# Optimization experiments

Measured on AMD Instinct MI355X. Metric: run time of the kernel, lower is better.

## Reference

```python
import jax, jax.numpy as jnp
import numpy as np

B, T, I, H, O = 2048, 512, 5, 64, 1


def setup_inputs() -> dict:
    key = jax.random.key(0)
    ks = jax.random.split(key, 11)
    s_ih0 = 1.0 / np.sqrt(H)
    def u(k, shape):
        return jax.random.uniform(k, shape, jnp.float32, -s_ih0, s_ih0)
    return {
        "x": jax.random.normal(ks[0], (B, T, I), jnp.float32),
        "W_ih0": u(ks[1], (H, I)),
        "W_hh0": u(ks[2], (H, H)),
        "b_ih0": u(ks[3], (H,)),
        "b_hh0": u(ks[4], (H,)),
        "W_ih1": u(ks[5], (H, H)),
        "W_hh1": u(ks[6], (H, H)),
        "b_ih1": u(ks[7], (H,)),
        "b_hh1": u(ks[8], (H,)),
        "fc_W": u(ks[9], (O, H)),
        "fc_b": u(ks[10], (O,)),
    }


def reference(x, W_ih0, W_hh0, b_ih0, b_hh0, W_ih1, W_hh1, b_ih1, b_hh1, fc_W, fc_b):
    # PyTorch RNN (tanh): h_t = tanh(x_t @ W_ih^T + b_ih + h_{t-1} @ W_hh^T + b_hh)
    # 2 stacked layers, h0 = zeros. Only last-timestep layer-2 output feeds fc.
    xT = jnp.swapaxes(x, 0, 1)  # [T, B, I]
    h0 = jnp.zeros((x.shape[0], H), x.dtype)

    def step(carry, x_t):
        h1, h2 = carry
        h1 = jnp.tanh(x_t @ W_ih0.T + b_ih0 + h1 @ W_hh0.T + b_hh0)
        h2 = jnp.tanh(h1 @ W_ih1.T + b_ih1 + h2 @ W_hh1.T + b_hh1)
        return (h1, h2), None

    (h1, h2), _ = jax.lax.scan(step, (h0, h0), xT)
    # out[:, -1, :] == final hidden state of top layer
    return h2 @ fc_W.T + fc_b
```

## Files before the change

kernel.cpp:

```cpp
#include <hip/hip_runtime.h>


constexpr int Bn = 2048;
constexpr int Tn = 512;
constexpr int In = 5;
constexpr int Hn = 64;

typedef _Float16 half4 __attribute__((ext_vector_type(4)));
typedef float f32x4 __attribute__((ext_vector_type(4)));

#define MFMA16(A, B, C) __builtin_amdgcn_mfma_f32_16x16x16f16((A), (B), (C), 0, 0, 0)

__device__ __forceinline__ unsigned pk(float a, float b) {
    union { _Float16 h[2]; unsigned u; } z;
    z.h[0] = (_Float16)a; z.h[1] = (_Float16)b;
    return z.u;
}
__device__ __forceinline__ half4 mkh4(unsigned a, unsigned b) {
    union { unsigned u[2]; half4 h; } z; z.u[0] = a; z.u[1] = b; return z.h;
}
__device__ __forceinline__ half4 h4of(unsigned long long v) {
    union { unsigned long long q; half4 h; } z; z.q = v; return z.h;
}

__device__ __forceinline__ float fast_tanh(float v) {
    v = __builtin_amdgcn_fmed3f(v, -15.f, 15.f);
    float e = __builtin_amdgcn_exp2f(v * 2.885390082f);
    return (e - 1.f) * __builtin_amdgcn_rcpf(e + 1.f);
}

__global__ __launch_bounds__(256) void rnn2_mfma4(
    const float* __restrict__ x,
    const float* __restrict__ W_ih0, const float* __restrict__ W_hh0,
    const float* __restrict__ b_ih0, const float* __restrict__ b_hh0,
    const float* __restrict__ W_ih1, const float* __restrict__ W_hh1,
    const float* __restrict__ b_ih1, const float* __restrict__ b_hh1,
    const float* __restrict__ fc_W, const float* __restrict__ fc_b,
    float* __restrict__ out)
{
    const int tid = threadIdx.x;
    const int w = tid >> 6;
    const int l = tid & 63;
    const int q = l >> 4, c = l & 15;
    const int b0 = blockIdx.x * 16;
    const int row = w * 16 + c;

    __shared__ unsigned long long h1buf[2][4][64];
    __shared__ unsigned long long h2buf[2][4][64];
    __shared__ float fcpart[4][16];

    half4 A_ih0;
    {
        unsigned a0 = 0, a1 = 0;
        const float* p = W_ih0 + row * In;
        if (q == 0)      { a0 = pk(p[0], p[1]); a1 = pk(p[2], p[3]); }
        else if (q == 1) { a0 = pk(p[4], 0.f); }
        A_ih0 = mkh4(a0, a1);
    }
    half4 A_hh0[4], A_ih1[4], A_hh1[4];
    #pragma unroll
    for (int kt = 0; kt < 4; ++kt) {
        const int off = row * Hn + kt * 16 + q * 4;
        float4 v0 = *reinterpret_cast<const float4*>(W_hh0 + off);
        A_hh0[kt] = mkh4(pk(v0.x, v0.y), pk(v0.z, v0.w));
        float4 v1 = *reinterpret_cast<const float4*>(W_ih1 + off);
        A_ih1[kt] = mkh4(pk(v1.x, v1.y), pk(v1.z, v1.w));
        float4 v2 = *reinterpret_cast<const float4*>(W_hh1 + off);
        A_hh1[kt] = mkh4(pk(v2.x, v2.y), pk(v2.z, v2.w));
    }

    f32x4 bc1, bc2;
    #pragma unroll
    for (int r = 0; r < 4; ++r) {
        const int rr = w * 16 + q * 4 + r;
        bc1[r] = b_ih0[rr] + b_hh0[rr];
        bc2[r] = b_ih1[rr] + b_hh1[rr];
    }

    unsigned long long h1B[4] = {0, 0, 0, 0};
    unsigned long long h2B[4] = {0, 0, 0, 0};
    f32x4 h2v = {0.f, 0.f, 0.f, 0.f};

    const float* xrow = x + (size_t)(b0 + c) * Tn * In;
    float nx0 = 0.f, nx1 = 0.f, nx2 = 0.f, nx3 = 0.f, nx4 = 0.f;
    if (q == 0)      { nx0 = xrow[0]; nx1 = xrow[1]; nx2 = xrow[2]; nx3 = xrow[3]; }
    else if (q == 1) { nx4 = xrow[4]; }

    #pragma unroll 1
    for (int t = 0; t < Tn; ++t) {
        unsigned r0 = (q == 0) ? pk(nx0, nx1) : ((q == 1) ? pk(nx4, 0.f) : 0u);
        unsigned r1 = (q == 0) ? pk(nx2, nx3) : 0u;
        const half4 XF = mkh4(r0, r1);

        const int tn = (t + 1 < Tn) ? (t + 1) : (Tn - 1);
        const float* xp = xrow + tn * In;
        if (q == 0)      { nx0 = xp[0]; nx1 = xp[1]; nx2 = xp[2]; nx3 = xp[3]; }
        else if (q == 1) { nx4 = xp[4]; }

        f32x4 acc = bc1;
        acc = MFMA16(A_ih0, XF, acc);
        #pragma unroll
        for (int kt = 0; kt < 4; ++kt)
            acc = MFMA16(A_hh0[kt], h4of(h1B[kt]), acc);
        float t0 = fast_tanh(acc[0]), t1 = fast_tanh(acc[1]);
        float t2 = fast_tanh(acc[2]), t3 = fast_tanh(acc[3]);
        unsigned long long myh1 =
            (unsigned long long)pk(t0, t1) | ((unsigned long long)pk(t2, t3) << 32);

        h1buf[t & 1][w][l] = myh1;
        __syncthreads();
        #pragma unroll
        for (int kt = 0; kt < 4; ++kt) h1B[kt] = h1buf[t & 1][kt][l];

        f32x4 aA = bc2;
        f32x4 aB = {0.f, 0.f, 0.f, 0.f};
        #pragma unroll
        for (int kt = 0; kt < 4; ++kt) {
            aA = MFMA16(A_ih1[kt], h4of(h1B[kt]), aA);
            aB = MFMA16(A_hh1[kt], h4of(h2B[kt]), aB);
        }
        h2v[0] = fast_tanh(aA[0] + aB[0]); h2v[1] = fast_tanh(aA[1] + aB[1]);
        h2v[2] = fast_tanh(aA[2] + aB[2]); h2v[3] = fast_tanh(aA[3] + aB[3]);
        unsigned long long myh2 =
            (unsigned long long)pk(h2v[0], h2v[1]) | ((unsigned long long)pk(h2v[2], h2v[3]) << 32);

        h2buf[t & 1][w][l] = myh2;
        __syncthreads();
        #pragma unroll
        for (int kt = 0; kt < 4; ++kt) h2B[kt] = h2buf[t & 1][kt][l];
    }

    float s = 0.f;
    #pragma unroll
    for (int e = 0; e < 4; ++e)
        s += fc_W[w * 16 + q * 4 + e] * h2v[e];
    s += __shfl_xor(s, 16, 64);
    s += __shfl_xor(s, 32, 64);
    if (l < 16) fcpart[w][l] = s;
    __syncthreads();
    if (tid < 16)
        out[b0 + tid] = fcpart[0][tid] + fcpart[1][tid] + fcpart[2][tid]
                      + fcpart[3][tid] + fc_b[0];
}

extern "C" void kernel_launch(void* const* d_in, const int* in_sizes, int n_in,
                              void* d_out, int out_size, void* d_ws, size_t ws_size,
                              hipStream_t stream) {
    const float* x     = (const float*)d_in[0];
    const float* W_ih0 = (const float*)d_in[1];
    const float* W_hh0 = (const float*)d_in[2];
    const float* b_ih0 = (const float*)d_in[3];
    const float* b_hh0 = (const float*)d_in[4];
    const float* W_ih1 = (const float*)d_in[5];
    const float* W_hh1 = (const float*)d_in[6];
    const float* b_ih1 = (const float*)d_in[7];
    const float* b_hh1 = (const float*)d_in[8];
    const float* fc_W  = (const float*)d_in[9];
    const float* fc_b  = (const float*)d_in[10];
    float* out = (float*)d_out;

    dim3 grid(Bn / 16);
    dim3 block(256);
    hipLaunchKernelGGL(rnn2_mfma4, grid, block, 0, stream,
                       x, W_ih0, W_hh0, b_ih0, b_hh0,
                       W_ih1, W_hh1, b_ih1, b_hh1, fc_W, fc_b, out);
}
```

Before: 360.9 us.

## Pipeline the two RNN layers across separate wave groups with one barrier per step

Splits each 512-thread block into two groups of four waves. One group computes layer 1 at step t while the other computes layer 2 at step t-1, so the two layers run concurrently with one barrier per iteration instead of two. MFMA accumulation chains are also split into independent partial sums to shorten the dependency chain. The cost is double the waves per block, an extra iteration, and divergent branches. Each block now holds twice as many threads, which may reduce how many blocks fit per CU.

```diff
diff --git a/kernel.cpp b/kernel.cpp
--- a/kernel.cpp
+++ b/kernel.cpp
@@ -29,7 +29,7 @@
     return (e - 1.f) * __builtin_amdgcn_rcpf(e + 1.f);
 }
 
-__global__ __launch_bounds__(256) void rnn2_mfma4(
+__global__ __launch_bounds__(512, 1) void rnn2_pipe(
     const float* __restrict__ x,
     const float* __restrict__ W_ih0, const float* __restrict__ W_hh0,
     const float* __restrict__ b_ih0, const float* __restrict__ b_hh0,
@@ -43,38 +43,49 @@
     const int l = tid & 63;
     const int q = l >> 4, c = l & 15;
     const int b0 = blockIdx.x * 16;
-    const int row = w * 16 + c;
+    const bool isL1 = (w < 4);
+    const int m = w & 3;
+    const int row = m * 16 + c;
 
     __shared__ unsigned long long h1buf[2][4][64];
     __shared__ unsigned long long h2buf[2][4][64];
     __shared__ float fcpart[4][16];
 
-    half4 A_ih0;
-    {
+    half4 A0 = mkh4(0u, 0u);
+    half4 AH[4], AI[4];
+    f32x4 bc;
+    if (isL1) {
         unsigned a0 = 0, a1 = 0;
         const float* p = W_ih0 + row * In;
         if (q == 0)      { a0 = pk(p[0], p[1]); a1 = pk(p[2], p[3]); }
         else if (q == 1) { a0 = pk(p[4], 0.f); }
-        A_ih0 = mkh4(a0, a1);
-    }
-    half4 A_hh0[4], A_ih1[4], A_hh1[4];
-    #pragma unroll
-    for (int kt = 0; kt < 4; ++kt) {
-        const int off = row * Hn + kt * 16 + q * 4;
-        float4 v0 = *reinterpret_cast<const float4*>(W_hh0 + off);
-        A_hh0[kt] = mkh4(pk(v0.x, v0.y), pk(v0.z, v0.w));
-        float4 v1 = *reinterpret_cast<const float4*>(W_ih1 + off);
-        A_ih1[kt] = mkh4(pk(v1.x, v1.y), pk(v1.z, v1.w));
-        float4 v2 = *reinterpret_cast<const float4*>(W_hh1 + off);
-        A_hh1[kt] = mkh4(pk(v2.x, v2.y), pk(v2.z, v2.w));
-    }
-
-    f32x4 bc1, bc2;
-    #pragma unroll
-    for (int r = 0; r < 4; ++r) {
-        const int rr = w * 16 + q * 4 + r;
-        bc1[r] = b_ih0[rr] + b_hh0[rr];
-        bc2[r] = b_ih1[rr] + b_hh1[rr];
+        A0 = mkh4(a0, a1);
+        #pragma unroll
+        for (int kt = 0; kt < 4; ++kt) {
+            const int off = row * Hn + kt * 16 + q * 4;
+            float4 v0 = *reinterpret_cast<const float4*>(W_hh0 + off);
+            AH[kt] = mkh4(pk(v0.x, v0.y), pk(v0.z, v0.w));
+            AI[kt] = mkh4(0u, 0u);
+        }
+        #pragma unroll
+        for (int r = 0; r < 4; ++r) {
+            const int rr = m * 16 + q * 4 + r;
+            bc[r] = b_ih0[rr] + b_hh0[rr];
+        }
+    } else {
+        #pragma unroll
+        for (int kt = 0; kt < 4; ++kt) {
+            const int off = row * Hn + kt * 16 + q * 4;
+            float4 v1 = *reinterpret_cast<const float4*>(W_ih1 + off);
+            AI[kt] = mkh4(pk(v1.x, v1.y), pk(v1.z, v1.w));
+            float4 v2 = *reinterpret_cast<const float4*>(W_hh1 + off);
+            AH[kt] = mkh4(pk(v2.x, v2.y), pk(v2.z, v2.w));
+        }
+        #pragma unroll
+        for (int r = 0; r < 4; ++r) {
+            const int rr = m * 16 + q * 4 + r;
+            bc[r] = b_ih1[rr] + b_hh1[rr];
+        }
     }
 
     unsigned long long h1B[4] = {0, 0, 0, 0};
@@ -83,60 +94,78 @@
 
     const float* xrow = x + (size_t)(b0 + c) * Tn * In;
     float nx0 = 0.f, nx1 = 0.f, nx2 = 0.f, nx3 = 0.f, nx4 = 0.f;
-    if (q == 0)      { nx0 = xrow[0]; nx1 = xrow[1]; nx2 = xrow[2]; nx3 = xrow[3]; }
-    else if (q == 1) { nx4 = xrow[4]; }
+    if (isL1) {
+        if (q == 0)      { nx0 = xrow[0]; nx1 = xrow[1]; nx2 = xrow[2]; nx3 = xrow[3]; }
+        else if (q == 1) { nx4 = xrow[4]; }
+    }
+
+    const f32x4 zero = {0.f, 0.f, 0.f, 0.f};
 
     #pragma unroll 1
-    for (int t = 0; t < Tn; ++t) {
-        unsigned r0 = (q == 0) ? pk(nx0, nx1) : ((q == 1) ? pk(nx4, 0.f) : 0u);
-        unsigned r1 = (q == 0) ? pk(nx2, nx3) : 0u;
-        const half4 XF = mkh4(r0, r1);
+    for (int t = 0; t <= Tn; ++t) {
+        if (isL1) {
+            if (t < Tn) {
+                unsigned r0 = (q == 0) ? pk(nx0, nx1) : ((q == 1) ? pk(nx4, 0.f) : 0u);
+                unsigned r1 = (q == 0) ? pk(nx2, nx3) : 0u;
+                const half4 XF = mkh4(r0, r1);
+                const int tn = (t + 1 < Tn) ? (t + 1) : (Tn - 1);
+                const float* xp = xrow + tn * In;
+                if (q == 0)      { nx0 = xp[0]; nx1 = xp[1]; nx2 = xp[2]; nx3 = xp[3]; }
+                else if (q == 1) { nx4 = xp[4]; }
 
-        const int tn = (t + 1 < Tn) ? (t + 1) : (Tn - 1);
-        const float* xp = xrow + tn * In;
-        if (q == 0)      { nx0 = xp[0]; nx1 = xp[1]; nx2 = xp[2]; nx3 = xp[3]; }
-        else if (q == 1) { nx4 = xp[4]; }
+                f32x4 cA = MFMA16(A0, XF, bc);
+                cA = MFMA16(AH[0], h4of(h1B[0]), cA);
+                f32x4 cB = MFMA16(AH[1], h4of(h1B[1]), zero);
+                cB = MFMA16(AH[2], h4of(h1B[2]), cB);
+                f32x4 cC = MFMA16(AH[3], h4of(h1B[3]), zero);
+                f32x4 s = (cA + cB) + cC;
+                float t0 = fast_tanh(s[0]), t1 = fast_tanh(s[1]);
+                float t2 = fast_tanh(s[2]), t3 = fast_tanh(s[3]);
+                h1buf[t & 1][m][l] =
+                    (unsigned long long)pk(t0, t1) | ((unsigned long long)pk(t2, t3) << 32);
+            }
+        } else {
+            if (t > 0) {
+                f32x4 aA = MFMA16(AI[0], h4of(h1B[0]), bc);
+                aA = MFMA16(AI[1], h4of(h1B[1]), aA);
+                f32x4 aB = MFMA16(AI[2], h4of(h1B[2]), zero);
+                aB = MFMA16(AI[3], h4of(h1B[3]), aB);
+                f32x4 aC = MFMA16(AH[0], h4of(h2B[0]), zero);
+                aC = MFMA16(AH[1], h4of(h2B[1]), aC);
+                f32x4 aD = MFMA16(AH[2], h4of(h2B[2]), zero);
+                aD = MFMA16(AH[3], h4of(h2B[3]), aD);
+                f32x4 s = (aA + aB) + (aC + aD);
+                h2v[0] = fast_tanh(s[0]); h2v[1] = fast_tanh(s[1]);
+                h2v[2] = fast_tanh(s[2]); h2v[3] = fast_tanh(s[3]);
+                h2buf[t & 1][m][l] =
+                    (unsigned long long)pk(h2v[0], h2v[1]) |
+                    ((unsigned long long)pk(h2v[2], h2v[3]) << 32);
+            } else {
+                h2buf[0][m][l] = 0ULL;
+            }
+        }
 
-        f32x4 acc = bc1;
-        acc = MFMA16(A_ih0, XF, acc);
-        #pragma unroll
-        for (int kt = 0; kt < 4; ++kt)
-            acc = MFMA16(A_hh0[kt], h4of(h1B[kt]), acc);
-        float t0 = fast_tanh(acc[0]), t1 = fast_tanh(acc[1]);
-        float t2 = fast_tanh(acc[2]), t3 = fast_tanh(acc[3]);
-        unsigned long long myh1 =
-            (unsigned long long)pk(t0, t1) | ((unsigned long long)pk(t2, t3) << 32);
+        __syncthreads();
 
-        h1buf[t & 1][w][l] = myh1;
-        __syncthreads();
-        #pragma unroll
-        for (int kt = 0; kt < 4; ++kt) h1B[kt] = h1buf[t & 1][kt][l];
-
-        f32x4 aA = bc2;
-        f32x4 aB = {0.f, 0.f, 0.f, 0.f};
-        #pragma unroll
-        for (int kt = 0; kt < 4; ++kt) {
-            aA = MFMA16(A_ih1[kt], h4of(h1B[kt]), aA);
-            aB = MFMA16(A_hh1[kt], h4of(h2B[kt]), aB);
+        if (t < Tn) {
+            #pragma unroll
+            for (int kt = 0; kt < 4; ++kt) h1B[kt] = h1buf[t & 1][kt][l];
         }
-        h2v[0] = fast_tanh(aA[0] + aB[0]); h2v[1] = fast_tanh(aA[1] + aB[1]);
-        h2v[2] = fast_tanh(aA[2] + aB[2]); h2v[3] = fast_tanh(aA[3] + aB[3]);
-        unsigned long long myh2 =
-            (unsigned long long)pk(h2v[0], h2v[1]) | ((unsigned long long)pk(h2v[2], h2v[3]) << 32);
-
-        h2buf[t & 1][w][l] = myh2;
-        __syncthreads();
-        #pragma unroll
-        for (int kt = 0; kt < 4; ++kt) h2B[kt] = h2buf[t & 1][kt][l];
+        if (!isL1) {
+            #pragma unroll
+            for (int kt = 0; kt < 4; ++kt) h2B[kt] = h2buf[t & 1][kt][l];
+        }
     }
 
-    float s = 0.f;
-    #pragma unroll
-    for (int e = 0; e < 4; ++e)
-        s += fc_W[w * 16 + q * 4 + e] * h2v[e];
-    s += __shfl_xor(s, 16, 64);
-    s += __shfl_xor(s, 32, 64);
-    if (l < 16) fcpart[w][l] = s;
+    if (!isL1) {
+        float s = 0.f;
+        #pragma unroll
+        for (int e = 0; e < 4; ++e)
+            s += fc_W[m * 16 + q * 4 + e] * h2v[e];
+        s += __shfl_xor(s, 16, 64);
+        s += __shfl_xor(s, 32, 64);
+        if (l < 16) fcpart[m][l] = s;
+    }
     __syncthreads();
     if (tid < 16)
         out[b0 + tid] = fcpart[0][tid] + fcpart[1][tid] + fcpart[2][tid]
@@ -160,8 +189,8 @@
     float* out = (float*)d_out;
 
     dim3 grid(Bn / 16);
-    dim3 block(256);
-    hipLaunchKernelGGL(rnn2_mfma4, grid, block, 0, stream,
+    dim3 block(512);
+    hipLaunchKernelGGL(rnn2_pipe, grid, block, 0, stream,
                        x, W_ih0, W_hh0, b_ih0, b_hh0,
                        W_ih1, W_hh1, b_ih1, b_hh1, fc_W, fc_b, out);
 }
```

Result: faster. 310.0 us (-14.1%).
